# Performance work log

Measured on AMD Instinct MI355X. Metric: run time of the kernel, lower is better.

The kernel has to match this reference:

```python
import jax, jax.numpy as jnp
import numpy as np

NUM_EMBEDDINGS = 512
EMBEDDING_DIM = 64


def setup_inputs() -> dict:
    key = jax.random.key(0)
    k_in, k_emb = jax.random.split(key)
    inputs = jax.random.normal(k_in, (8, 64, 16, 32, 32), dtype=jnp.float32)
    # matches torch uniform_(-1/K, 1/K) init
    lim = 1.0 / NUM_EMBEDDINGS
    embedding = jax.random.uniform(
        k_emb, (NUM_EMBEDDINGS, EMBEDDING_DIM), dtype=jnp.float32,
        minval=-lim, maxval=lim)
    return {"inputs": inputs, "embedding": embedding}


def reference(inputs, embedding):
    # inputs: (B, C=D, T, H, W); embedding: (K, D)
    x = jnp.transpose(inputs, (0, 2, 3, 4, 1))  # (B, T, H, W, D)
    in_shape = x.shape
    flat = x.reshape(-1, EMBEDDING_DIM)  # (N, D)
    distances = (
        jnp.sum(flat * flat, axis=1, keepdims=True)
        + jnp.sum(embedding * embedding, axis=1)
        - 2.0 * jnp.matmul(flat, embedding.T)
    )  # (N, K)
    # NOTE: original applies softmax to raw (positive) distances, faithfully kept
    weights = jax.nn.softmax(distances, axis=1)
    out = jnp.matmul(weights, embedding).reshape(in_shape)  # (B,T,H,W,D)
    return jnp.transpose(out, (0, 4, 1, 2, 3))  # (B, D, T, H, W)
```

## Files before the change

### kernel.cpp

```cpp
#include <hip/hip_runtime.h>
#include <hip/hip_bf16.h>

typedef __attribute__((ext_vector_type(8))) short short8;
typedef __attribute__((ext_vector_type(4))) short short4v;
typedef __attribute__((ext_vector_type(4))) _Float16 half4;
typedef __attribute__((ext_vector_type(4))) float f32x4;

#define SPW 16384
#define XST 72
#define LOG2E 1.4426950408889634f

__device__ __forceinline__ float exp2_hw(float f) {
  return __builtin_amdgcn_exp2f(f);
}

__device__ __forceinline__ short bf16s(float f) {
  union { __hip_bfloat16 h; short s; } u;
  u.h = __float2bfloat16(f);
  return u.s;
}

__global__ void prep_all(const float* __restrict__ emb, short8* __restrict__ a1,
                         half4* __restrict__ eb, float* __restrict__ norms) {
  const int f = blockIdx.x * 256 + threadIdx.x;
  if (f < 4096) {
    const int l = f & 63;
    const int s = (f >> 6) & 1;
    const int m = f >> 7;
    const int row = m * 16 + (l & 15);
    const int col0 = s * 32 + (l >> 4) * 8;
    short8 v;
    #pragma unroll
    for (int i = 0; i < 8; ++i)
      v[i] = bf16s(-2.0f * LOG2E * emb[row * 64 + col0 + i]);
    a1[f] = v;
  } else if (f < 12288) {
    const int e = f - 4096;
    const int l = e & 63;
    const int m2 = (e >> 6) & 3;
    const int kt = e >> 8;
    const int d = m2 * 16 + (l & 15);
    const int k0 = kt * 16 + 4 * (l >> 4);
    half4 v;
    #pragma unroll
    for (int i = 0; i < 4; ++i) v[i] = (_Float16)emb[(k0 + i) * 64 + d];
    eb[e] = v;
  } else if (f < 12800) {
    const int k = f - 12288;
    float acc = 0.f;
    #pragma unroll
    for (int d = 0; d < 64; ++d) { float e = emb[k * 64 + d]; acc += e * e; }
    norms[k] = acc * LOG2E;
  }
}

__global__ __launch_bounds__(64, 4) void vq_main(
    const float* __restrict__ x, const short8* __restrict__ a1,
    const half4* __restrict__ eb, const float* __restrict__ norms,
    float* __restrict__ out) {
  __shared__ __align__(16) short Xl[32 * XST];
  __shared__ float dl[32];

  const int lane = threadIdx.x;
  const int l15 = lane & 15;
  const int g = lane >> 4;

  const int tile = blockIdx.x * 32;
  const int b = tile >> 14;
  const int off = tile & 16383;
  const float* xb = x + (size_t)b * (64 * SPW) + off;
  float* ob = out + (size_t)b * (64 * SPW) + off;

  {
    const int l8 = lane & 7;
    const int lh = lane >> 3;
    const int n0 = 4 * l8;
    const int sw = l8 << 3;
    #pragma unroll
    for (int h = 0; h < 2; ++h) {
      const int d0 = lh * 8 + h * 4;
      const float4 r0 = *reinterpret_cast<const float4*>(xb + (size_t)(d0 + 0) * SPW + n0);
      const float4 r1 = *reinterpret_cast<const float4*>(xb + (size_t)(d0 + 1) * SPW + n0);
      const float4 r2 = *reinterpret_cast<const float4*>(xb + (size_t)(d0 + 2) * SPW + n0);
      const float4 r3 = *reinterpret_cast<const float4*>(xb + (size_t)(d0 + 3) * SPW + n0);
      const short4v c0 = {bf16s(r0.x), bf16s(r1.x), bf16s(r2.x), bf16s(r3.x)};
      const short4v c1 = {bf16s(r0.y), bf16s(r1.y), bf16s(r2.y), bf16s(r3.y)};
      const short4v c2 = {bf16s(r0.z), bf16s(r1.z), bf16s(r2.z), bf16s(r3.z)};
      const short4v c3 = {bf16s(r0.w), bf16s(r1.w), bf16s(r2.w), bf16s(r3.w)};
      const int dsw = d0 ^ sw;
      *reinterpret_cast<short4v*>(&Xl[(n0 + 0) * XST + dsw]) = c0;
      *reinterpret_cast<short4v*>(&Xl[(n0 + 1) * XST + dsw]) = c1;
      *reinterpret_cast<short4v*>(&Xl[(n0 + 2) * XST + dsw]) = c2;
      *reinterpret_cast<short4v*>(&Xl[(n0 + 3) * XST + dsw]) = c3;
    }
  }
  __syncthreads();

  short8 bx[2][2];
  #pragma unroll
  for (int j = 0; j < 2; ++j) {
    const int n = j * 16 + l15;
    const int swn = ((n >> 2) & 7) << 3;
    bx[j][0] = *reinterpret_cast<const short8*>(&Xl[n * XST + ((g * 8) ^ swn)]);
    bx[j][1] = *reinterpret_cast<const short8*>(&Xl[n * XST + ((32 + g * 8) ^ swn)]);
  }

  f32x4 pacc[2][4];
  #pragma unroll
  for (int j = 0; j < 2; ++j)
    #pragma unroll
    for (int m2 = 0; m2 < 4; ++m2) pacc[j][m2] = f32x4{0.f, 0.f, 0.f, 0.f};
  float denp[2] = {0.f, 0.f};

  for (int c = 0; c < 8; ++c) {
    #pragma unroll 2
    for (int q = 0; q < 4; ++q) {
      const int kt = c * 4 + q;
      const short8 a1f0 = a1[(kt * 2 + 0) * 64 + lane];
      const short8 a1f1 = a1[(kt * 2 + 1) * 64 + lane];
      const half4 e0 = eb[(kt * 4 + 0) * 64 + lane];
      const half4 e1 = eb[(kt * 4 + 1) * 64 + lane];
      const half4 e2 = eb[(kt * 4 + 2) * 64 + lane];
      const half4 e3 = eb[(kt * 4 + 3) * 64 + lane];
      const float4 nv = *reinterpret_cast<const float4*>(&norms[kt * 16 + g * 4]);
      #pragma unroll
      for (int j = 0; j < 2; ++j) {
        f32x4 z = {0.f, 0.f, 0.f, 0.f};
        z = __builtin_amdgcn_mfma_f32_16x16x32_bf16(a1f0, bx[j][0], z, 0, 0, 0);
        z = __builtin_amdgcn_mfma_f32_16x16x32_bf16(a1f1, bx[j][1], z, 0, 0, 0);
        const float p0 = exp2_hw(nv.x + z[0]);
        const float p1 = exp2_hw(nv.y + z[1]);
        const float p2 = exp2_hw(nv.z + z[2]);
        const float p3 = exp2_hw(nv.w + z[3]);
        denp[j] += (p0 + p1) + (p2 + p3);
        const half4 pa = {(_Float16)p0, (_Float16)p1, (_Float16)p2, (_Float16)p3};
        pacc[j][0] = __builtin_amdgcn_mfma_f32_16x16x16f16(pa, e0, pacc[j][0], 0, 0, 0);
        pacc[j][1] = __builtin_amdgcn_mfma_f32_16x16x16f16(pa, e1, pacc[j][1], 0, 0, 0);
        pacc[j][2] = __builtin_amdgcn_mfma_f32_16x16x16f16(pa, e2, pacc[j][2], 0, 0, 0);
        pacc[j][3] = __builtin_amdgcn_mfma_f32_16x16x16f16(pa, e3, pacc[j][3], 0, 0, 0);
      }
    }
  }

  #pragma unroll
  for (int j = 0; j < 2; ++j) {
    denp[j] += __shfl_xor(denp[j], 16, 64);
    denp[j] += __shfl_xor(denp[j], 32, 64);
  }
  if (lane < 16) {
    dl[lane] = denp[0];
    dl[16 + lane] = denp[1];
  }
  __syncthreads();
  const float4 dA = *reinterpret_cast<const float4*>(&dl[4 * g]);
  const float4 dB = *reinterpret_cast<const float4*>(&dl[16 + 4 * g]);
  const f32x4 rd0 = {1.0f / dA.x, 1.0f / dA.y, 1.0f / dA.z, 1.0f / dA.w};
  const f32x4 rd1 = {1.0f / dB.x, 1.0f / dB.y, 1.0f / dB.z, 1.0f / dB.w};

  #pragma unroll
  for (int j = 0; j < 2; ++j) {
    const f32x4 rd = j ? rd1 : rd0;
    const int nbase = j * 16 + 4 * g;
    #pragma unroll
    for (int m2 = 0; m2 < 4; ++m2) {
      const f32x4 s = pacc[j][m2];
      const float4 o = {s[0] * rd[0], s[1] * rd[1], s[2] * rd[2], s[3] * rd[3]};
      const int d = m2 * 16 + l15;
      *reinterpret_cast<float4*>(&ob[(size_t)d * SPW + nbase]) = o;
    }
  }
}

extern "C" void kernel_launch(void* const* d_in, const int* in_sizes, int n_in,
                              void* d_out, int out_size, void* d_ws, size_t ws_size,
                              hipStream_t stream) {
  (void)in_sizes; (void)n_in; (void)out_size; (void)ws_size;
  const float* x   = (const float*)d_in[0];
  const float* emb = (const float*)d_in[1];
  float* out = (float*)d_out;

  char* ws = (char*)d_ws;
  short8* a1   = (short8*)ws;
  half4*  eb   = (half4*)(ws + 65536);
  float*  norms = (float*)(ws + 131072);

  prep_all<<<50, 256, 0, stream>>>(emb, a1, eb, norms);
  vq_main<<<4096, 64, 0, stream>>>(x, a1, eb, norms, out);
}
```

Measured before the change: 46.63 us.

## Split codebook across four waves per block with LDS cross-wave reduction

```diff
diff --git a/kernel.cpp b/kernel.cpp
--- a/kernel.cpp
+++ b/kernel.cpp
@@ -8,6 +8,7 @@
 
 #define SPW 16384
 #define XST 72
+#define RW  66
 #define LOG2E 1.4426950408889634f
 
 __device__ __forceinline__ float exp2_hw(float f) {
@@ -54,14 +55,18 @@
   }
 }
 
-__global__ __launch_bounds__(64, 4) void vq_main(
+__global__ __launch_bounds__(256, 4) void vq_main(
     const float* __restrict__ x, const short8* __restrict__ a1,
     const half4* __restrict__ eb, const float* __restrict__ norms,
     float* __restrict__ out) {
-  __shared__ __align__(16) short Xl[32 * XST];
-  __shared__ float dl[32];
+  __shared__ __align__(16) char lds_raw[17408];
+  short* Xl   = reinterpret_cast<short*>(lds_raw);
+  float* Rf   = reinterpret_cast<float*>(lds_raw);
+  float* denl = reinterpret_cast<float*>(lds_raw + 16896);
 
-  const int lane = threadIdx.x;
+  const int t = threadIdx.x;
+  const int lane = t & 63;
+  const int w = t >> 6;
   const int l15 = lane & 15;
   const int g = lane >> 4;
 
@@ -71,38 +76,30 @@
   const float* xb = x + (size_t)b * (64 * SPW) + off;
   float* ob = out + (size_t)b * (64 * SPW) + off;
 
-  {
-    const int l8 = lane & 7;
-    const int lh = lane >> 3;
-    const int n0 = 4 * l8;
-    const int sw = l8 << 3;
-    #pragma unroll
-    for (int h = 0; h < 2; ++h) {
-      const int d0 = lh * 8 + h * 4;
-      const float4 r0 = *reinterpret_cast<const float4*>(xb + (size_t)(d0 + 0) * SPW + n0);
-      const float4 r1 = *reinterpret_cast<const float4*>(xb + (size_t)(d0 + 1) * SPW + n0);
-      const float4 r2 = *reinterpret_cast<const float4*>(xb + (size_t)(d0 + 2) * SPW + n0);
-      const float4 r3 = *reinterpret_cast<const float4*>(xb + (size_t)(d0 + 3) * SPW + n0);
-      const short4v c0 = {bf16s(r0.x), bf16s(r1.x), bf16s(r2.x), bf16s(r3.x)};
-      const short4v c1 = {bf16s(r0.y), bf16s(r1.y), bf16s(r2.y), bf16s(r3.y)};
-      const short4v c2 = {bf16s(r0.z), bf16s(r1.z), bf16s(r2.z), bf16s(r3.z)};
-      const short4v c3 = {bf16s(r0.w), bf16s(r1.w), bf16s(r2.w), bf16s(r3.w)};
-      const int dsw = d0 ^ sw;
-      *reinterpret_cast<short4v*>(&Xl[(n0 + 0) * XST + dsw]) = c0;
-      *reinterpret_cast<short4v*>(&Xl[(n0 + 1) * XST + dsw]) = c1;
-      *reinterpret_cast<short4v*>(&Xl[(n0 + 2) * XST + dsw]) = c2;
-      *reinterpret_cast<short4v*>(&Xl[(n0 + 3) * XST + dsw]) = c3;
-    }
+  if (t < 128) {
+    const int n0 = 4 * (t & 7);
+    const int d0 = 4 * (t >> 3);
+    const float4 r0 = *reinterpret_cast<const float4*>(xb + (size_t)(d0 + 0) * SPW + n0);
+    const float4 r1 = *reinterpret_cast<const float4*>(xb + (size_t)(d0 + 1) * SPW + n0);
+    const float4 r2 = *reinterpret_cast<const float4*>(xb + (size_t)(d0 + 2) * SPW + n0);
+    const float4 r3 = *reinterpret_cast<const float4*>(xb + (size_t)(d0 + 3) * SPW + n0);
+    const short4v c0 = {bf16s(r0.x), bf16s(r1.x), bf16s(r2.x), bf16s(r3.x)};
+    const short4v c1 = {bf16s(r0.y), bf16s(r1.y), bf16s(r2.y), bf16s(r3.y)};
+    const short4v c2 = {bf16s(r0.z), bf16s(r1.z), bf16s(r2.z), bf16s(r3.z)};
+    const short4v c3 = {bf16s(r0.w), bf16s(r1.w), bf16s(r2.w), bf16s(r3.w)};
+    *reinterpret_cast<short4v*>(&Xl[(n0 + 0) * XST + d0]) = c0;
+    *reinterpret_cast<short4v*>(&Xl[(n0 + 1) * XST + d0]) = c1;
+    *reinterpret_cast<short4v*>(&Xl[(n0 + 2) * XST + d0]) = c2;
+    *reinterpret_cast<short4v*>(&Xl[(n0 + 3) * XST + d0]) = c3;
   }
   __syncthreads();
 
   short8 bx[2][2];
   #pragma unroll
   for (int j = 0; j < 2; ++j) {
-    const int n = j * 16 + l15;
-    const int swn = ((n >> 2) & 7) << 3;
-    bx[j][0] = *reinterpret_cast<const short8*>(&Xl[n * XST + ((g * 8) ^ swn)]);
-    bx[j][1] = *reinterpret_cast<const short8*>(&Xl[n * XST + ((32 + g * 8) ^ swn)]);
+    const int base = (j * 16 + l15) * XST + g * 8;
+    bx[j][0] = *reinterpret_cast<const short8*>(&Xl[base]);
+    bx[j][1] = *reinterpret_cast<const short8*>(&Xl[base + 32]);
   }
 
   f32x4 pacc[2][4];
@@ -112,33 +109,31 @@
     for (int m2 = 0; m2 < 4; ++m2) pacc[j][m2] = f32x4{0.f, 0.f, 0.f, 0.f};
   float denp[2] = {0.f, 0.f};
 
-  for (int c = 0; c < 8; ++c) {
-    #pragma unroll 2
-    for (int q = 0; q < 4; ++q) {
-      const int kt = c * 4 + q;
-      const short8 a1f0 = a1[(kt * 2 + 0) * 64 + lane];
-      const short8 a1f1 = a1[(kt * 2 + 1) * 64 + lane];
-      const half4 e0 = eb[(kt * 4 + 0) * 64 + lane];
-      const half4 e1 = eb[(kt * 4 + 1) * 64 + lane];
-      const half4 e2 = eb[(kt * 4 + 2) * 64 + lane];
-      const half4 e3 = eb[(kt * 4 + 3) * 64 + lane];
-      const float4 nv = *reinterpret_cast<const float4*>(&norms[kt * 16 + g * 4]);
-      #pragma unroll
-      for (int j = 0; j < 2; ++j) {
-        f32x4 z = {0.f, 0.f, 0.f, 0.f};
-        z = __builtin_amdgcn_mfma_f32_16x16x32_bf16(a1f0, bx[j][0], z, 0, 0, 0);
-        z = __builtin_amdgcn_mfma_f32_16x16x32_bf16(a1f1, bx[j][1], z, 0, 0, 0);
-        const float p0 = exp2_hw(nv.x + z[0]);
-        const float p1 = exp2_hw(nv.y + z[1]);
-        const float p2 = exp2_hw(nv.z + z[2]);
-        const float p3 = exp2_hw(nv.w + z[3]);
-        denp[j] += (p0 + p1) + (p2 + p3);
-        const half4 pa = {(_Float16)p0, (_Float16)p1, (_Float16)p2, (_Float16)p3};
-        pacc[j][0] = __builtin_amdgcn_mfma_f32_16x16x16f16(pa, e0, pacc[j][0], 0, 0, 0);
-        pacc[j][1] = __builtin_amdgcn_mfma_f32_16x16x16f16(pa, e1, pacc[j][1], 0, 0, 0);
-        pacc[j][2] = __builtin_amdgcn_mfma_f32_16x16x16f16(pa, e2, pacc[j][2], 0, 0, 0);
-        pacc[j][3] = __builtin_amdgcn_mfma_f32_16x16x16f16(pa, e3, pacc[j][3], 0, 0, 0);
-      }
+  #pragma unroll 2
+  for (int q = 0; q < 8; ++q) {
+    const int kt = w * 8 + q;
+    const short8 a1f0 = a1[(kt * 2 + 0) * 64 + lane];
+    const short8 a1f1 = a1[(kt * 2 + 1) * 64 + lane];
+    const half4 e0 = eb[(kt * 4 + 0) * 64 + lane];
+    const half4 e1 = eb[(kt * 4 + 1) * 64 + lane];
+    const half4 e2 = eb[(kt * 4 + 2) * 64 + lane];
+    const half4 e3 = eb[(kt * 4 + 3) * 64 + lane];
+    const float4 nv = *reinterpret_cast<const float4*>(&norms[kt * 16 + g * 4]);
+    #pragma unroll
+    for (int j = 0; j < 2; ++j) {
+      f32x4 z = {0.f, 0.f, 0.f, 0.f};
+      z = __builtin_amdgcn_mfma_f32_16x16x32_bf16(a1f0, bx[j][0], z, 0, 0, 0);
+      z = __builtin_amdgcn_mfma_f32_16x16x32_bf16(a1f1, bx[j][1], z, 0, 0, 0);
+      const float p0 = exp2_hw(nv.x + z[0]);
+      const float p1 = exp2_hw(nv.y + z[1]);
+      const float p2 = exp2_hw(nv.z + z[2]);
+      const float p3 = exp2_hw(nv.w + z[3]);
+      denp[j] += (p0 + p1) + (p2 + p3);
+      const half4 pa = {(_Float16)p0, (_Float16)p1, (_Float16)p2, (_Float16)p3};
+      pacc[j][0] = __builtin_amdgcn_mfma_f32_16x16x16f16(pa, e0, pacc[j][0], 0, 0, 0);
+      pacc[j][1] = __builtin_amdgcn_mfma_f32_16x16x16f16(pa, e1, pacc[j][1], 0, 0, 0);
+      pacc[j][2] = __builtin_amdgcn_mfma_f32_16x16x16f16(pa, e2, pacc[j][2], 0, 0, 0);
+      pacc[j][3] = __builtin_amdgcn_mfma_f32_16x16x16f16(pa, e3, pacc[j][3], 0, 0, 0);
     }
   }
 
@@ -148,25 +143,30 @@
     denp[j] += __shfl_xor(denp[j], 32, 64);
   }
   if (lane < 16) {
-    dl[lane] = denp[0];
-    dl[16 + lane] = denp[1];
+    denl[w * 32 + l15] = denp[0];
+    denl[w * 32 + 16 + l15] = denp[1];
   }
-  __syncthreads();
-  const float4 dA = *reinterpret_cast<const float4*>(&dl[4 * g]);
-  const float4 dB = *reinterpret_cast<const float4*>(&dl[16 + 4 * g]);
-  const f32x4 rd0 = {1.0f / dA.x, 1.0f / dA.y, 1.0f / dA.z, 1.0f / dA.w};
-  const f32x4 rd1 = {1.0f / dB.x, 1.0f / dB.y, 1.0f / dB.z, 1.0f / dB.w};
 
+  const int n16 = t & 15;
+  const int dq2 = t >> 4;
   #pragma unroll
   for (int j = 0; j < 2; ++j) {
-    const f32x4 rd = j ? rd1 : rd0;
-    const int nbase = j * 16 + 4 * g;
+    __syncthreads();
     #pragma unroll
-    for (int m2 = 0; m2 < 4; ++m2) {
-      const f32x4 s = pacc[j][m2];
-      const float4 o = {s[0] * rd[0], s[1] * rd[1], s[2] * rd[2], s[3] * rd[3]};
-      const int d = m2 * 16 + l15;
-      *reinterpret_cast<float4*>(&ob[(size_t)d * SPW + nbase]) = o;
+    for (int m2 = 0; m2 < 4; ++m2)
+      #pragma unroll
+      for (int r = 0; r < 4; ++r)
+        Rf[(w * 16 + 4 * g + r) * RW + m2 * 16 + l15] = pacc[j][m2][r];
+    __syncthreads();
+    const float den = (denl[j * 16 + n16] + denl[32 + j * 16 + n16])
+                    + (denl[64 + j * 16 + n16] + denl[96 + j * 16 + n16]);
+    const float rdv = 1.0f / den;
+    #pragma unroll
+    for (int r = 0; r < 4; ++r) {
+      const int dd = r * 16 + dq2;
+      const float sum = (Rf[n16 * RW + dd] + Rf[(16 + n16) * RW + dd])
+                      + (Rf[(32 + n16) * RW + dd] + Rf[(48 + n16) * RW + dd]);
+      ob[(size_t)dd * SPW + j * 16 + n16] = sum * rdv;
     }
   }
 }
@@ -185,5 +185,5 @@
   float*  norms = (float*)(ws + 131072);
 
   prep_all<<<50, 256, 0, stream>>>(emb, a1, eb, norms);
-  vq_main<<<4096, 64, 0, stream>>>(x, a1, eb, norms, out);
+  vq_main<<<4096, 256, 0, stream>>>(x, a1, eb, norms, out);
 }
```

Measured after the change: 45.43 us. -2.6%, faster.
